# Optimization experiments

Measured on AMD Instinct MI355X. Metric: run time of the kernel, lower is better.

## Reference

```python
import jax, jax.numpy as jnp
import numpy as np

GW_EPS = 0.05
GW_SIGMA = 1.0
GW_OUTER_ITERS = 5
GW_SINK_ITERS = 20
N_HEADS = 8
EPS = 1e-8


def normalize_affinity(P):
    # symmetrize, scale to [0,1]
    P = 0.5 * (P + jnp.swapaxes(P, -1, -2))
    mx = jnp.max(P, axis=(-2, -1), keepdims=True)
    return P / jnp.maximum(mx, EPS)


def entropic_gw(C1, C2, a, b, eps, outer_iters, sink_iters):
    # C1: [B,H,S,S] node-space cost, C2: [B,H,K,K] slot-space cost
    # a: [B,H,S], b: [B,H,K] marginals. Square-loss entropic GW (Peyre et al.)
    T = a[..., :, None] * b[..., None, :]                      # [B,H,S,K]
    cC1 = jnp.einsum('bhij,bhj->bhi', C1 * C1, a)              # [B,H,S]
    cC2 = jnp.einsum('bhk,bhkl->bhl', b, C2 * C2)              # [B,H,K]
    const = cC1[..., :, None] + cC2[..., None, :]              # [B,H,S,K]
    tens = const
    for _ in range(outer_iters):
        tens = const - 2.0 * jnp.einsum('bhis,bhsk,bhlk->bhil', C1, T, C2)
        Kmat = jnp.exp(-tens / eps)
        u = jnp.ones_like(a)
        v = jnp.ones_like(b)
        def sink_step(carry, _):
            u, v = carry
            u = a / jnp.maximum(jnp.einsum('bhik,bhk->bhi', Kmat, v), 1e-30)
            v = b / jnp.maximum(jnp.einsum('bhik,bhi->bhk', Kmat, u), 1e-30)
            return (u, v), None
        (u, v), _ = jax.lax.scan(sink_step, (u, v), None, length=sink_iters)
        T = u[..., :, None] * Kmat * v[..., None, :]
    gw_val = jnp.sum(tens * T, axis=(-2, -1))                  # [B,H]
    return T, gw_val


def _forward(desc_embeddings, name_value_embeddings, shared_attn, prior_Q, DG, b, v_w, v_b):
    B, new_seq, D = name_value_embeddings.shape
    S = new_seq - 1
    H = N_HEADS
    hd = D // H

    # structural adjacency: CLS->Var on, Var->CLS off, Var-Var without self-loop
    var_adj = 1.0 - jnp.eye(S, dtype=name_value_embeddings.dtype)
    adj = jnp.zeros((new_seq, new_seq), dtype=name_value_embeddings.dtype)
    adj = adj.at[1:, 1:].set(var_adj)
    adj = adj.at[0, 1:].set(1.0)

    # Var-Var affinity from shared attention (detached in original)
    P_var = jax.lax.stop_gradient(shared_attn[:, :, 1:, 1:])   # [B,H,S,S]
    P_norm = normalize_affinity(P_var)
    DP = 1.0 - P_norm                                          # affinity -> distance

    deg_P = 0.5 * (P_norm.sum(-1) + P_norm.sum(-2))            # [B,H,S]
    a = deg_P / jnp.maximum(deg_P.sum(-1, keepdims=True), EPS)

    _, gw_val = entropic_gw(DP, DG, a, b, GW_EPS, GW_OUTER_ITERS, GW_SINK_ITERS)
    alpha = jnp.exp(-gw_val / GW_SIGMA)                        # [B,H] in (0,1]

    # sharpen prior Q by alpha (power sharpening + row renorm)
    Q_hat = jnp.power(jnp.maximum(prior_Q, EPS), 1.0 + alpha[..., None, None])
    Q_hat = Q_hat / jnp.maximum(Q_hat.sum(-1, keepdims=True), EPS)

    # embed Q_hat into CLS-augmented attention, mask, row-normalize
    slot = jnp.zeros((B, H, new_seq, new_seq), dtype=Q_hat.dtype)
    slot = slot.at[:, :, 1:, 1:].set(Q_hat)
    slot = slot.at[:, :, 0, 1:].set(1.0)
    slot = slot * adj[None, None]
    attn = slot / jnp.maximum(slot.sum(-1, keepdims=True), EPS)  # [B,H,S1,S1]

    v = name_value_embeddings @ v_w.T + v_b                    # [B,S1,D]
    v = v.reshape(B, new_seq, H, hd).transpose(0, 2, 1, 3)     # [B,H,S1,hd]
    context = jnp.einsum('bhij,bhjd->bhid', attn, v)
    basis_outputs = context.transpose(0, 2, 1, 3)              # [B,S1,H,hd]
    return basis_outputs, attn


def setup_inputs() -> dict:
    key = jax.random.key(0)
    ks = jax.random.split(key, 8)
    B, S1, D, H, K = 32, 385, 256, 8, 16
    S = S1 - 1
    desc = jax.random.normal(ks[0], (B, S, D), jnp.float32)
    nv = jax.random.normal(ks[1], (B, S1, D), jnp.float32)
    shared_attn = jax.nn.softmax(jax.random.normal(ks[2], (B, H, S1, S1), jnp.float32), axis=-1)
    prior_Q = jax.nn.softmax(jax.random.normal(ks[3], (B, H, S, S), jnp.float32), axis=-1)
    DG = jax.random.uniform(ks[4], (B, H, K, K), jnp.float32)
    DG = 0.5 * (DG + jnp.swapaxes(DG, -1, -2))
    b = jax.random.uniform(ks[5], (B, H, K), jnp.float32) + 0.1
    b = b / b.sum(-1, keepdims=True)
    v_w = jax.random.normal(ks[6], (D, D), jnp.float32) * (1.0 / np.sqrt(D))
    v_b = jnp.zeros((D,), jnp.float32)
    return {"desc_embeddings": desc, "name_value_embeddings": nv, "shared_attn": shared_attn,
            "prior_Q": prior_Q, "DG": DG, "b": b, "v_w": v_w, "v_b": v_b}


def reference(desc_embeddings, name_value_embeddings, shared_attn, prior_Q, DG, b, v_w, v_b):
    return _forward(desc_embeddings, name_value_embeddings, shared_attn, prior_Q, DG, b, v_w, v_b)
```

## Files before the change

kernel.cpp:

```cpp
#include <hip/hip_runtime.h>
#include <math.h>

constexpr int kS  = 384;
constexpr int kS1 = 385;
constexpr int kH  = 8;
constexpr int kB  = 32;
constexpr int kD  = 256;
constexpr float kEPS = 1e-8f;
constexpr float kNEG_INV_EPS_LOG2E = 28.853900817779268f;

__device__ __forceinline__ float waveReduceSum(float v) {
    #pragma unroll
    for (int m = 1; m < 64; m <<= 1) v += __shfl_xor(v, m);
    return v;
}
__device__ __forceinline__ float waveReduceMax(float v) {
    #pragma unroll
    for (int m = 1; m < 64; m <<= 1) v = fmaxf(v, __shfl_xor(v, m));
    return v;
}

__global__ __launch_bounds__(384) void k1_gw(
    const float* __restrict__ shared_attn,
    const float* __restrict__ DG,
    const float* __restrict__ bmarg,
    float* __restrict__ sym_ws,
    float* __restrict__ alpha_out)
{
    const int head = blockIdx.x;
    const int tid  = threadIdx.x;
    const int lane = tid & 63, wid = tid >> 6;

    __shared__ __align__(16) float uni[8320];
    __shared__ float Ks[kS * 17];
    __shared__ float ravu[kS];
    __shared__ float part[16 * 24];
    __shared__ float C2l[256];
    __shared__ float bl16[16], cb16[16], cC216[16], vls[16];
    __shared__ float wred[6];

    float* tA = uni;
    float* tB = uni + 4160;
    float* Ms = uni;

    const float* P = shared_attn + (size_t)head * (kS1 * kS1);
    float* SYM = sym_ws + (size_t)head * (kS1 * kS1);

    ravu[tid] = 0.f;
    if (tid < 256) C2l[tid] = DG[head * 256 + tid];
    if (tid >= 256 && tid < 272) bl16[tid - 256] = bmarg[head * 16 + (tid - 256)];
    __syncthreads();

    float mymax = -1e30f;
    for (int ti = 0; ti < 6; ++ti)
    for (int tj = ti; tj < 6; ++tj) {
        for (int e = tid; e < 4096; e += 384) {
            int r = e >> 6, c = e & 63;
            tA[r * 65 + c] = P[(ti * 64 + r + 1) * kS1 + (tj * 64 + c + 1)];
            tB[r * 65 + c] = P[(tj * 64 + r + 1) * kS1 + (ti * 64 + c + 1)];
        }
        __syncthreads();
        for (int e = tid; e < 4096; e += 384) {
            int r = e >> 6, c = e & 63;
            float v = 0.5f * (tA[r * 65 + c] + tB[c * 65 + r]);
            tA[r * 65 + c] = v;
            mymax = fmaxf(mymax, v);
        }
        __syncthreads();
        for (int e = tid; e < 4096; e += 384) {
            int r = e >> 6, c = e & 63;
            SYM[(ti * 64 + r) * kS + tj * 64 + c] = tA[r * 65 + c];
        }
        if (ti != tj) {
            for (int e = tid; e < 4096; e += 384) {
                int r = e >> 6, c = e & 63;
                SYM[(tj * 64 + r) * kS + ti * 64 + c] = tA[c * 65 + r];
            }
        }
        if (tid < 64) {
            int r = tid; float s = 0.f;
            #pragma unroll 8
            for (int c = 0; c < 64; ++c) s += tA[r * 65 + c];
            ravu[ti * 64 + r] += s;
        } else if (tid < 128 && ti != tj) {
            int c = tid - 64; float s = 0.f;
            #pragma unroll 8
            for (int r = 0; r < 64; ++r) s += tA[r * 65 + c];
            ravu[tj * 64 + c] += s;
        }
        __syncthreads();
    }

    float wm = waveReduceMax(mymax);
    if (lane == 0) wred[wid] = wm;
    __syncthreads();
    const float mx = fmaxf(fmaxf(fmaxf(wred[0], wred[1]), fmaxf(wred[2], wred[3])),
                           fmaxf(wred[4], wred[5]));
    float tloc = ravu[tid];
    float tw = waveReduceSum(tloc);
    __syncthreads();
    if (lane == 0) wred[wid] = tw;
    __syncthreads();
    const float total = wred[0] + wred[1] + wred[2] + wred[3] + wred[4] + wred[5];

    const float den_mx = fmaxf(mx, kEPS);
    const float inv_mx = 1.0f / den_mx;
    const float Sdeg   = total * inv_mx;
    const float den_a  = fmaxf(Sdeg, kEPS);
    const float a_reg  = (tloc * inv_mx) / den_a;
    __syncthreads();
    ravu[tid] = a_reg;

    if (tid < 16) {
        float cb = 0.f, cc2 = 0.f;
        #pragma unroll
        for (int k = 0; k < 16; ++k) {
            cb += bl16[k] * C2l[tid * 16 + k];
            float c2 = C2l[k * 16 + tid];
            cc2 = fmaf(bl16[k] * c2, c2, cc2);
        }
        cb16[tid] = cb; cC216[tid] = cc2;
    }
    __syncthreads();

    float t1 = 0.f, t2 = 0.f;
    {
        const float* symcol = SYM + tid;
        #pragma unroll 4
        for (int s = 0; s < kS; ++s) {
            float sym = symcol[s * kS];
            float dp  = fmaf(-inv_mx, sym, 1.0f);
            float as  = ravu[s];
            t1 = fmaf(dp, as, t1);
            t2 = fmaf(dp * dp, as, t2);
        }
    }
    const float cc1 = t2;
    #pragma unroll
    for (int l = 0; l < 16; ++l) {
        float tens = cc1 + cC216[l] - 2.0f * cb16[l] * t1;
        Ks[tid * 17 + l] = exp2f(tens * (-kNEG_INV_EPS_LOG2E));
    }

    float vreg[16];
    float u_i = 0.f;

    auto sinkhorn = [&]() {
        #pragma unroll
        for (int l = 0; l < 16; ++l) vreg[l] = 1.0f;
        for (int it = 0; it < 20; ++it) {
            float su = 0.f;
            #pragma unroll
            for (int l = 0; l < 16; ++l) su = fmaf(Ks[tid * 17 + l], vreg[l], su);
            u_i = a_reg / fmaxf(su, 1e-30f);
            ravu[tid] = u_i;
            __syncthreads();
            {
                int l = tid & 15, g = tid >> 4;
                float sv = 0.f;
                #pragma unroll
                for (int j = 0; j < 16; ++j)
                    sv = fmaf(Ks[(g * 16 + j) * 17 + l], ravu[g * 16 + j], sv);
                part[l * 24 + g] = sv;
            }
            __syncthreads();
            if (tid < 16) {
                float dn = 0.f;
                #pragma unroll
                for (int g = 0; g < 24; ++g) dn += part[tid * 24 + g];
                vls[tid] = bl16[tid] / fmaxf(dn, 1e-30f);
            }
            __syncthreads();
            #pragma unroll
            for (int l = 0; l < 16; ++l) vreg[l] = vls[l];
        }
    };

    __syncthreads();
    sinkhorn();

    float tens16[16];
    #pragma unroll
    for (int l = 0; l < 16; ++l) tens16[l] = 0.f;

    for (int outer = 1; outer < 5; ++outer) {
        {
            float wk[16];
            #pragma unroll
            for (int k = 0; k < 16; ++k) wk[k] = Ks[tid * 17 + k] * vreg[k];
            float m[16];
            #pragma unroll
            for (int l = 0; l < 16; ++l) {
                float acc = 0.f;
                #pragma unroll
                for (int k = 0; k < 16; ++k) acc = fmaf(wk[k], C2l[l * 16 + k], acc);
                m[l] = acc * u_i;
            }
            float4* Ms4 = (float4*)Ms;
            Ms4[tid * 4 + 0] = make_float4(m[0],  m[1],  m[2],  m[3]);
            Ms4[tid * 4 + 1] = make_float4(m[4],  m[5],  m[6],  m[7]);
            Ms4[tid * 4 + 2] = make_float4(m[8],  m[9],  m[10], m[11]);
            Ms4[tid * 4 + 3] = make_float4(m[12], m[13], m[14], m[15]);
        }
        __syncthreads();
        float rd[16];
        #pragma unroll
        for (int l = 0; l < 16; ++l) rd[l] = 0.f;
        {
            const float* symcol = SYM + tid;
            const float4* Ms4 = (const float4*)Ms;
            #pragma unroll 2
            for (int s = 0; s < kS; ++s) {
                float sym = symcol[s * kS];
                float dp  = fmaf(-inv_mx, sym, 1.0f);
                float4 m0 = Ms4[s * 4 + 0];
                float4 m1 = Ms4[s * 4 + 1];
                float4 m2 = Ms4[s * 4 + 2];
                float4 m3 = Ms4[s * 4 + 3];
                rd[0]  = fmaf(dp, m0.x, rd[0]);  rd[1]  = fmaf(dp, m0.y, rd[1]);
                rd[2]  = fmaf(dp, m0.z, rd[2]);  rd[3]  = fmaf(dp, m0.w, rd[3]);
                rd[4]  = fmaf(dp, m1.x, rd[4]);  rd[5]  = fmaf(dp, m1.y, rd[5]);
                rd[6]  = fmaf(dp, m1.z, rd[6]);  rd[7]  = fmaf(dp, m1.w, rd[7]);
                rd[8]  = fmaf(dp, m2.x, rd[8]);  rd[9]  = fmaf(dp, m2.y, rd[9]);
                rd[10] = fmaf(dp, m2.z, rd[10]); rd[11] = fmaf(dp, m2.w, rd[11]);
                rd[12] = fmaf(dp, m3.x, rd[12]); rd[13] = fmaf(dp, m3.y, rd[13]);
                rd[14] = fmaf(dp, m3.z, rd[14]); rd[15] = fmaf(dp, m3.w, rd[15]);
            }
        }
        #pragma unroll
        for (int l = 0; l < 16; ++l) {
            float tens = cc1 + cC216[l] - 2.0f * rd[l];
            if (outer == 4) tens16[l] = tens;
            Ks[tid * 17 + l] = exp2f(tens * (-kNEG_INV_EPS_LOG2E));
        }
        __syncthreads();
        sinkhorn();
    }

    float g = 0.f;
    #pragma unroll
    for (int l = 0; l < 16; ++l)
        g = fmaf(tens16[l] * Ks[tid * 17 + l], vreg[l], g);
    g *= u_i;
    float gww = waveReduceSum(g);
    __syncthreads();
    if (lane == 0) wred[wid] = gww;
    __syncthreads();
    if (tid == 0) {
        float gw = wred[0] + wred[1] + wred[2] + wred[3] + wred[4] + wred[5];
        alpha_out[head] = expf(-gw);
    }
}

__global__ __launch_bounds__(256) void k2_attn(
    const float* __restrict__ priorQ,
    const float* __restrict__ alpha_in,
    float* __restrict__ attn_out)
{
    const int tid  = threadIdx.x;
    const int lane = tid & 63, wid = tid >> 6;
    const int head = blockIdx.x / 97;
    const int i    = (blockIdx.x % 97) * 4 + wid;
    if (i >= kS1) return;
    float* row = attn_out + (size_t)head * (kS1 * kS1) + (size_t)i * kS1;
    if (i == 0) {
        const float val = 1.0f / 384.0f;
        for (int j = lane; j < kS1; j += 64) row[j] = (j == 0) ? 0.f : val;
        return;
    }
    const float e = 1.0f + alpha_in[head];
    const float* q = priorQ + (size_t)head * (kS * kS) + (size_t)(i - 1) * kS;
    float p[6];
    float loc = 0.f, locd = 0.f;
    #pragma unroll
    for (int k = 0; k < 6; ++k) {
        int j = lane + k * 64;
        float qv = fmaxf(q[j], kEPS);
        float pv = exp2f(e * log2f(qv));
        p[k] = pv;
        loc += pv;
        if (j == i - 1) locd = pv;
    }
    float sum = loc, pd = locd;
    #pragma unroll
    for (int m = 1; m < 64; m <<= 1) { sum += __shfl_xor(sum, m); pd += __shfl_xor(pd, m); }
    const float qsum  = fmaxf(sum, kEPS);
    const float srow  = (sum - pd) / qsum;
    const float scale = 1.0f / (qsum * fmaxf(srow, kEPS));
    if (lane == 0) row[0] = 0.f;
    #pragma unroll
    for (int k = 0; k < 6; ++k) {
        int j = lane + k * 64;
        row[1 + j] = (j == i - 1) ? 0.f : p[k] * scale;
    }
}

__global__ __launch_bounds__(256) void k3_vproj(
    const float* __restrict__ nv,
    const float* __restrict__ vw,
    const float* __restrict__ vb,
    float* __restrict__ vfull)
{
    __shared__ float At[64][17];
    __shared__ float Bt[256][17];
    const int tid = threadIdx.x;
    const int r0  = blockIdx.x * 64;
    const int tx  = tid & 31;
    const int ty  = tid >> 5;
    const int M   = kB * kS1;
    float acc[8][8];
    #pragma unroll
    for (int ri = 0; ri < 8; ++ri)
        #pragma unroll
        for (int ci = 0; ci < 8; ++ci) acc[ri][ci] = 0.f;

    for (int k0 = 0; k0 < 256; k0 += 16) {
        __syncthreads();
        for (int e = tid; e < 1024; e += 256) {
            int r = e >> 4, kk = e & 15;
            int rowi = r0 + r;
            At[r][kk] = (rowi < M) ? nv[rowi * 256 + k0 + kk] : 0.f;
        }
        for (int e = tid; e < 4096; e += 256) {
            int c = e >> 4, kk = e & 15;
            Bt[c][kk] = vw[c * 256 + k0 + kk];
        }
        __syncthreads();
        #pragma unroll
        for (int kk = 0; kk < 16; ++kk) {
            float av[8], bv[8];
            #pragma unroll
            for (int ri = 0; ri < 8; ++ri) av[ri] = At[ty * 8 + ri][kk];
            #pragma unroll
            for (int ci = 0; ci < 8; ++ci) bv[ci] = Bt[tx + 32 * ci][kk];
            #pragma unroll
            for (int ri = 0; ri < 8; ++ri)
                #pragma unroll
                for (int ci = 0; ci < 8; ++ci)
                    acc[ri][ci] = fmaf(av[ri], bv[ci], acc[ri][ci]);
        }
    }
    for (int ri = 0; ri < 8; ++ri) {
        int rowi = r0 + ty * 8 + ri;
        if (rowi < M) {
            #pragma unroll
            for (int ci = 0; ci < 8; ++ci) {
                int c = tx + 32 * ci;
                vfull[rowi * 256 + c] = acc[ri][ci] + vb[c];
            }
        }
    }
}

__global__ __launch_bounds__(256) void k4_ctx(
    const float* __restrict__ attn,
    const float* __restrict__ vfull,
    float* __restrict__ basis)
{
    __shared__ __align__(16) float at[8 * 32 * 28];
    __shared__ float vt[24 * 256];
    const int tid = threadIdx.x;
    const int bb  = blockIdx.y;
    const int i0  = blockIdx.x * 32;
    const int h   = tid >> 5;
    float acc[32];
    #pragma unroll
    for (int i = 0; i < 32; ++i) acc[i] = 0.f;
    const float* attnB = attn + (size_t)bb * kH * kS1 * kS1;
    const float* vB    = vfull + (size_t)bb * kS1 * 256;

    for (int j0 = 0; j0 < kS1; j0 += 24) {
        __syncthreads();
        for (int e = tid; e < 6144; e += 256) {
            int jj = e % 24, ii = (e / 24) & 31, hh = e / (24 * 32);
            int gi = i0 + ii, gj = j0 + jj;
            float v = (gi < kS1 && gj < kS1)
                      ? attnB[(size_t)hh * kS1 * kS1 + (size_t)gi * kS1 + gj] : 0.f;
            at[(hh * 32 + ii) * 28 + jj] = v;
        }
        for (int e = tid; e < 6144; e += 256) {
            int c = e & 255, jr = e >> 8;
            int gj = j0 + jr;
            vt[jr * 256 + c] = (gj < kS1) ? vB[gj * 256 + c] : 0.f;
        }
        __syncthreads();
        #pragma unroll
        for (int j4 = 0; j4 < 6; ++j4) {
            float v0 = vt[(j4 * 4 + 0) * 256 + tid];
            float v1 = vt[(j4 * 4 + 1) * 256 + tid];
            float v2 = vt[(j4 * 4 + 2) * 256 + tid];
            float v3 = vt[(j4 * 4 + 3) * 256 + tid];
            #pragma unroll
            for (int i = 0; i < 32; ++i) {
                float4 av = *(const float4*)&at[(h * 32 + i) * 28 + j4 * 4];
                acc[i] = fmaf(av.x, v0, fmaf(av.y, v1, fmaf(av.z, v2, fmaf(av.w, v3, acc[i]))));
            }
        }
    }
    for (int i = 0; i < 32; ++i) {
        int gi = i0 + i;
        if (gi < kS1) basis[((size_t)bb * kS1 + gi) * 256 + tid] = acc[i];
    }
}

extern "C" void kernel_launch(void* const* d_in, const int* in_sizes, int n_in,
                              void* d_out, int out_size, void* d_ws, size_t ws_size,
                              hipStream_t stream) {
    (void)in_sizes; (void)n_in; (void)out_size; (void)ws_size;
    const float* nv    = (const float*)d_in[1];
    const float* sattn = (const float*)d_in[2];
    const float* pq    = (const float*)d_in[3];
    const float* dg    = (const float*)d_in[4];
    const float* bm    = (const float*)d_in[5];
    const float* vw    = (const float*)d_in[6];
    const float* vb    = (const float*)d_in[7];

    float* out   = (float*)d_out;
    float* basis = out;
    float* attn  = out + (size_t)kB * kS1 * kD;
    float* alpha = (float*)d_ws;
    float* vfull = (float*)((char*)d_ws + 4096);

    k1_gw<<<256, 384, 0, stream>>>(sattn, dg, bm, attn, alpha);
    k2_attn<<<256 * 97, 256, 0, stream>>>(pq, alpha, attn);
    k3_vproj<<<193, 256, 0, stream>>>(nv, vw, vb, vfull);
    k4_ctx<<<dim3(13, 32), 256, 0, stream>>>(attn, vfull, basis);
}
```

Measured before the change: 1.334 ms.

## Split GW symmetrization into parallel kernel, keep Sinkhorn kernel in registers, retile context

Symmetrizing the affinity matrix, along with its row sums and max, moves out of the per-head GW kernel into a separate kernel launched with six blocks per head, so that phase no longer runs on only 256 blocks. The GW kernel now holds the Gibbs kernel in registers and reduces the Sinkhorn column sums with wave shuffles instead of a shared-memory pass. It also reads SYM rows as float4 rather than strided columns, which relies on SYM being symmetric and on a per-head alignment offset. Separately, the context kernel uses 16-row tiles for more blocks and loads V with float4. The cost is an extra launch plus storing and re-reading the sums and max through global memory.

New measurement: 1.322 ms. About the same (-0.9%).

```diff
diff --git a/kernel.cpp b/kernel.cpp
--- a/kernel.cpp
+++ b/kernel.cpp
@@ -20,8 +20,63 @@
     return v;
 }
 
-__global__ __launch_bounds__(384) void k1_gw(
+__device__ __forceinline__ size_t symBase(int head) {
+    return (size_t)head * (kS1 * kS1) + (size_t)((4 - (head & 3)) & 3);
+}
+
+__global__ __launch_bounds__(256) void k1a_sym(
     const float* __restrict__ shared_attn,
+    float* __restrict__ sym_ws)
+{
+    const int head = blockIdx.y;
+    const int ti   = blockIdx.x;
+    const int tid  = threadIdx.x;
+    const int c    = tid & 63;
+    const int w    = tid >> 6;
+
+    __shared__ float tB[64 * 65];
+    __shared__ float wredA[4];
+
+    const float* P = shared_attn + (size_t)head * (kS1 * kS1);
+    float* SYM = sym_ws + symBase(head);
+    float* rs  = SYM + kS * kS;
+    float* mxs = rs + kS;
+
+    float rs_part[16];
+    #pragma unroll
+    for (int k = 0; k < 16; ++k) rs_part[k] = 0.f;
+    float mymax = 0.f;
+
+    for (int tj = 0; tj < 6; ++tj) {
+        __syncthreads();
+        for (int e = tid; e < 4096; e += 256) {
+            int r = e >> 6, cc = e & 63;
+            tB[r * 65 + cc] = P[(size_t)(1 + tj * 64 + r) * kS1 + (1 + ti * 64 + cc)];
+        }
+        __syncthreads();
+        #pragma unroll
+        for (int k = 0; k < 16; ++k) {
+            int r = w + 4 * k;
+            float av = P[(size_t)(1 + ti * 64 + r) * kS1 + (1 + tj * 64 + c)];
+            float v  = 0.5f * (av + tB[c * 65 + r]);
+            mymax = fmaxf(mymax, v);
+            rs_part[k] += v;
+            SYM[(size_t)(ti * 64 + r) * kS + tj * 64 + c] = v;
+        }
+    }
+    #pragma unroll
+    for (int k = 0; k < 16; ++k) {
+        float s = waveReduceSum(rs_part[k]);
+        if (c == 0) rs[ti * 64 + w + 4 * k] = s;
+    }
+    float wm = waveReduceMax(mymax);
+    if (c == 0) wredA[w] = wm;
+    __syncthreads();
+    if (tid == 0)
+        mxs[ti] = fmaxf(fmaxf(wredA[0], wredA[1]), fmaxf(wredA[2], wredA[3]));
+}
+
+__global__ __launch_bounds__(384) void k1b_gw(
     const float* __restrict__ DG,
     const float* __restrict__ bmarg,
     float* __restrict__ sym_ws,
@@ -31,84 +86,32 @@
     const int tid  = threadIdx.x;
     const int lane = tid & 63, wid = tid >> 6;
 
-    __shared__ __align__(16) float uni[8320];
-    __shared__ float Ks[kS * 17];
+    __shared__ __align__(16) float Ms[kS * 16];
     __shared__ float ravu[kS];
-    __shared__ float part[16 * 24];
+    __shared__ float part[6 * 16];
     __shared__ float C2l[256];
     __shared__ float bl16[16], cb16[16], cC216[16], vls[16];
     __shared__ float wred[6];
 
-    float* tA = uni;
-    float* tB = uni + 4160;
-    float* Ms = uni;
-
-    const float* P = shared_attn + (size_t)head * (kS1 * kS1);
-    float* SYM = sym_ws + (size_t)head * (kS1 * kS1);
-
-    ravu[tid] = 0.f;
+    float* SYM = sym_ws + symBase(head);
+    const float* rs  = SYM + kS * kS;
+    const float* mxp = rs + kS;
+
     if (tid < 256) C2l[tid] = DG[head * 256 + tid];
     if (tid >= 256 && tid < 272) bl16[tid - 256] = bmarg[head * 16 + (tid - 256)];
-    __syncthreads();
-
-    float mymax = -1e30f;
-    for (int ti = 0; ti < 6; ++ti)
-    for (int tj = ti; tj < 6; ++tj) {
-        for (int e = tid; e < 4096; e += 384) {
-            int r = e >> 6, c = e & 63;
-            tA[r * 65 + c] = P[(ti * 64 + r + 1) * kS1 + (tj * 64 + c + 1)];
-            tB[r * 65 + c] = P[(tj * 64 + r + 1) * kS1 + (ti * 64 + c + 1)];
-        }
-        __syncthreads();
-        for (int e = tid; e < 4096; e += 384) {
-            int r = e >> 6, c = e & 63;
-            float v = 0.5f * (tA[r * 65 + c] + tB[c * 65 + r]);
-            tA[r * 65 + c] = v;
-            mymax = fmaxf(mymax, v);
-        }
-        __syncthreads();
-        for (int e = tid; e < 4096; e += 384) {
-            int r = e >> 6, c = e & 63;
-            SYM[(ti * 64 + r) * kS + tj * 64 + c] = tA[r * 65 + c];
-        }
-        if (ti != tj) {
-            for (int e = tid; e < 4096; e += 384) {
-                int r = e >> 6, c = e & 63;
-                SYM[(tj * 64 + r) * kS + ti * 64 + c] = tA[c * 65 + r];
-            }
-        }
-        if (tid < 64) {
-            int r = tid; float s = 0.f;
-            #pragma unroll 8
-            for (int c = 0; c < 64; ++c) s += tA[r * 65 + c];
-            ravu[ti * 64 + r] += s;
-        } else if (tid < 128 && ti != tj) {
-            int c = tid - 64; float s = 0.f;
-            #pragma unroll 8
-            for (int r = 0; r < 64; ++r) s += tA[r * 65 + c];
-            ravu[tj * 64 + c] += s;
-        }
-        __syncthreads();
-    }
-
-    float wm = waveReduceMax(mymax);
-    if (lane == 0) wred[wid] = wm;
-    __syncthreads();
-    const float mx = fmaxf(fmaxf(fmaxf(wred[0], wred[1]), fmaxf(wred[2], wred[3])),
-                           fmaxf(wred[4], wred[5]));
-    float tloc = ravu[tid];
+
+    const float tloc = rs[tid];
     float tw = waveReduceSum(tloc);
-    __syncthreads();
     if (lane == 0) wred[wid] = tw;
     __syncthreads();
     const float total = wred[0] + wred[1] + wred[2] + wred[3] + wred[4] + wred[5];
-
+    const float mx = fmaxf(fmaxf(fmaxf(mxp[0], mxp[1]), fmaxf(mxp[2], mxp[3])),
+                           fmaxf(mxp[4], mxp[5]));
     const float den_mx = fmaxf(mx, kEPS);
     const float inv_mx = 1.0f / den_mx;
     const float Sdeg   = total * inv_mx;
     const float den_a  = fmaxf(Sdeg, kEPS);
     const float a_reg  = (tloc * inv_mx) / den_a;
-    __syncthreads();
     ravu[tid] = a_reg;
 
     if (tid < 16) {
@@ -123,27 +126,25 @@
     }
     __syncthreads();
 
+    const float4* __restrict__ symrow = (const float4*)(SYM + (size_t)tid * kS);
     float t1 = 0.f, t2 = 0.f;
-    {
-        const float* symcol = SYM + tid;
-        #pragma unroll 4
-        for (int s = 0; s < kS; ++s) {
-            float sym = symcol[s * kS];
-            float dp  = fmaf(-inv_mx, sym, 1.0f);
-            float as  = ravu[s];
-            t1 = fmaf(dp, as, t1);
-            t2 = fmaf(dp * dp, as, t2);
-        }
+    #pragma unroll 4
+    for (int s4 = 0; s4 < 96; ++s4) {
+        float4 v4 = symrow[s4];
+        const float* av = &ravu[s4 * 4];
+        float dp;
+        dp = fmaf(-inv_mx, v4.x, 1.0f); t1 = fmaf(dp, av[0], t1); t2 = fmaf(dp * dp, av[0], t2);
+        dp = fmaf(-inv_mx, v4.y, 1.0f); t1 = fmaf(dp, av[1], t1); t2 = fmaf(dp * dp, av[1], t2);
+        dp = fmaf(-inv_mx, v4.z, 1.0f); t1 = fmaf(dp, av[2], t1); t2 = fmaf(dp * dp, av[2], t2);
+        dp = fmaf(-inv_mx, v4.w, 1.0f); t1 = fmaf(dp, av[3], t1); t2 = fmaf(dp * dp, av[3], t2);
     }
     const float cc1 = t2;
-    #pragma unroll
-    for (int l = 0; l < 16; ++l) {
-        float tens = cc1 + cC216[l] - 2.0f * cb16[l] * t1;
-        Ks[tid * 17 + l] = exp2f(tens * (-kNEG_INV_EPS_LOG2E));
-    }
-
-    float vreg[16];
+
+    float kreg[16], vreg[16];
     float u_i = 0.f;
+    #pragma unroll
+    for (int l = 0; l < 16; ++l)
+        kreg[l] = exp2f((cc1 + cC216[l] - 2.0f * cb16[l] * t1) * (-kNEG_INV_EPS_LOG2E));
 
     auto sinkhorn = [&]() {
         #pragma unroll
@@ -151,23 +152,17 @@
         for (int it = 0; it < 20; ++it) {
             float su = 0.f;
             #pragma unroll
-            for (int l = 0; l < 16; ++l) su = fmaf(Ks[tid * 17 + l], vreg[l], su);
+            for (int l = 0; l < 16; ++l) su = fmaf(kreg[l], vreg[l], su);
             u_i = a_reg / fmaxf(su, 1e-30f);
-            ravu[tid] = u_i;
-            __syncthreads();
-            {
-                int l = tid & 15, g = tid >> 4;
-                float sv = 0.f;
-                #pragma unroll
-                for (int j = 0; j < 16; ++j)
-                    sv = fmaf(Ks[(g * 16 + j) * 17 + l], ravu[g * 16 + j], sv);
-                part[l * 24 + g] = sv;
+            #pragma unroll
+            for (int l = 0; l < 16; ++l) {
+                float t = waveReduceSum(kreg[l] * u_i);
+                if (lane == 0) part[wid * 16 + l] = t;
             }
             __syncthreads();
             if (tid < 16) {
-                float dn = 0.f;
-                #pragma unroll
-                for (int g = 0; g < 24; ++g) dn += part[tid * 24 + g];
+                float dn = part[tid] + part[16 + tid] + part[32 + tid] +
+                           part[48 + tid] + part[64 + tid] + part[80 + tid];
                 vls[tid] = bl16[tid] / fmaxf(dn, 1e-30f);
             }
             __syncthreads();
@@ -176,7 +171,6 @@
         }
     };
 
-    __syncthreads();
     sinkhorn();
 
     float tens16[16];
@@ -187,7 +181,7 @@
         {
             float wk[16];
             #pragma unroll
-            for (int k = 0; k < 16; ++k) wk[k] = Ks[tid * 17 + k] * vreg[k];
+            for (int k = 0; k < 16; ++k) wk[k] = kreg[k] * vreg[k];
             float m[16];
             #pragma unroll
             for (int l = 0; l < 16; ++l) {
@@ -196,54 +190,55 @@
                 for (int k = 0; k < 16; ++k) acc = fmaf(wk[k], C2l[l * 16 + k], acc);
                 m[l] = acc * u_i;
             }
-            float4* Ms4 = (float4*)Ms;
-            Ms4[tid * 4 + 0] = make_float4(m[0],  m[1],  m[2],  m[3]);
-            Ms4[tid * 4 + 1] = make_float4(m[4],  m[5],  m[6],  m[7]);
-            Ms4[tid * 4 + 2] = make_float4(m[8],  m[9],  m[10], m[11]);
-            Ms4[tid * 4 + 3] = make_float4(m[12], m[13], m[14], m[15]);
+            float4* Ms4w = (float4*)Ms;
+            Ms4w[tid * 4 + 0] = make_float4(m[0],  m[1],  m[2],  m[3]);
+            Ms4w[tid * 4 + 1] = make_float4(m[4],  m[5],  m[6],  m[7]);
+            Ms4w[tid * 4 + 2] = make_float4(m[8],  m[9],  m[10], m[11]);
+            Ms4w[tid * 4 + 3] = make_float4(m[12], m[13], m[14], m[15]);
         }
         __syncthreads();
         float rd[16];
         #pragma unroll
         for (int l = 0; l < 16; ++l) rd[l] = 0.f;
         {
-            const float* symcol = SYM + tid;
             const float4* Ms4 = (const float4*)Ms;
             #pragma unroll 2
-            for (int s = 0; s < kS; ++s) {
-                float sym = symcol[s * kS];
-                float dp  = fmaf(-inv_mx, sym, 1.0f);
-                float4 m0 = Ms4[s * 4 + 0];
-                float4 m1 = Ms4[s * 4 + 1];
-                float4 m2 = Ms4[s * 4 + 2];
-                float4 m3 = Ms4[s * 4 + 3];
-                rd[0]  = fmaf(dp, m0.x, rd[0]);  rd[1]  = fmaf(dp, m0.y, rd[1]);
-                rd[2]  = fmaf(dp, m0.z, rd[2]);  rd[3]  = fmaf(dp, m0.w, rd[3]);
-                rd[4]  = fmaf(dp, m1.x, rd[4]);  rd[5]  = fmaf(dp, m1.y, rd[5]);
-                rd[6]  = fmaf(dp, m1.z, rd[6]);  rd[7]  = fmaf(dp, m1.w, rd[7]);
-                rd[8]  = fmaf(dp, m2.x, rd[8]);  rd[9]  = fmaf(dp, m2.y, rd[9]);
-                rd[10] = fmaf(dp, m2.z, rd[10]); rd[11] = fmaf(dp, m2.w, rd[11]);
-                rd[12] = fmaf(dp, m3.x, rd[12]); rd[13] = fmaf(dp, m3.y, rd[13]);
-                rd[14] = fmaf(dp, m3.z, rd[14]); rd[15] = fmaf(dp, m3.w, rd[15]);
+            for (int s4 = 0; s4 < 96; ++s4) {
+                float4 v4 = symrow[s4];
+                #pragma unroll
+                for (int j = 0; j < 4; ++j) {
+                    float sym = (j == 0) ? v4.x : (j == 1) ? v4.y : (j == 2) ? v4.z : v4.w;
+                    float dp = fmaf(-inv_mx, sym, 1.0f);
+                    const int s = s4 * 4 + j;
+                    float4 m0 = Ms4[s * 4 + 0];
+                    float4 m1 = Ms4[s * 4 + 1];
+                    float4 m2 = Ms4[s * 4 + 2];
+                    float4 m3 = Ms4[s * 4 + 3];
+                    rd[0]  = fmaf(dp, m0.x, rd[0]);  rd[1]  = fmaf(dp, m0.y, rd[1]);
+                    rd[2]  = fmaf(dp, m0.z, rd[2]);  rd[3]  = fmaf(dp, m0.w, rd[3]);
+                    rd[4]  = fmaf(dp, m1.x, rd[4]);  rd[5]  = fmaf(dp, m1.y, rd[5]);
+                    rd[6]  = fmaf(dp, m1.z, rd[6]);  rd[7]  = fmaf(dp, m1.w, rd[7]);
+                    rd[8]  = fmaf(dp, m2.x, rd[8]);  rd[9]  = fmaf(dp, m2.y, rd[9]);
+                    rd[10] = fmaf(dp, m2.z, rd[10]); rd[11] = fmaf(dp, m2.w, rd[11]);
+                    rd[12] = fmaf(dp, m3.x, rd[12]); rd[13] = fmaf(dp, m3.y, rd[13]);
+                    rd[14] = fmaf(dp, m3.z, rd[14]); rd[15] = fmaf(dp, m3.w, rd[15]);
+                }
             }
         }
         #pragma unroll
         for (int l = 0; l < 16; ++l) {
             float tens = cc1 + cC216[l] - 2.0f * rd[l];
             if (outer == 4) tens16[l] = tens;
-            Ks[tid * 17 + l] = exp2f(tens * (-kNEG_INV_EPS_LOG2E));
-        }
-        __syncthreads();
+            kreg[l] = exp2f(tens * (-kNEG_INV_EPS_LOG2E));
+        }
         sinkhorn();
     }
 
     float g = 0.f;
     #pragma unroll
-    for (int l = 0; l < 16; ++l)
-        g = fmaf(tens16[l] * Ks[tid * 17 + l], vreg[l], g);
+    for (int l = 0; l < 16; ++l) g = fmaf(tens16[l] * kreg[l], vreg[l], g);
     g *= u_i;
     float gww = waveReduceSum(g);
-    __syncthreads();
     if (lane == 0) wred[wid] = gww;
     __syncthreads();
     if (tid == 0) {
@@ -357,47 +352,49 @@
     const float* __restrict__ vfull,
     float* __restrict__ basis)
 {
-    __shared__ __align__(16) float at[8 * 32 * 28];
-    __shared__ float vt[24 * 256];
+    __shared__ __align__(16) float at[8 * 16 * 36];
+    __shared__ __align__(16) float vt[32 * 256];
     const int tid = threadIdx.x;
     const int bb  = blockIdx.y;
-    const int i0  = blockIdx.x * 32;
+    const int i0  = blockIdx.x * 16;
     const int h   = tid >> 5;
-    float acc[32];
-    #pragma unroll
-    for (int i = 0; i < 32; ++i) acc[i] = 0.f;
+    float acc[16];
+    #pragma unroll
+    for (int i = 0; i < 16; ++i) acc[i] = 0.f;
     const float* attnB = attn + (size_t)bb * kH * kS1 * kS1;
     const float* vB    = vfull + (size_t)bb * kS1 * 256;
 
-    for (int j0 = 0; j0 < kS1; j0 += 24) {
-        __syncthreads();
-        for (int e = tid; e < 6144; e += 256) {
-            int jj = e % 24, ii = (e / 24) & 31, hh = e / (24 * 32);
+    for (int j0 = 0; j0 < kS1; j0 += 32) {
+        __syncthreads();
+        for (int e = tid; e < 4096; e += 256) {
+            int jj = e & 31, ii = (e >> 5) & 15, hh = e >> 9;
             int gi = i0 + ii, gj = j0 + jj;
-            float v = (gi < kS1 && gj < kS1)
-                      ? attnB[(size_t)hh * kS1 * kS1 + (size_t)gi * kS1 + gj] : 0.f;
-            at[(hh * 32 + ii) * 28 + jj] = v;
-        }
-        for (int e = tid; e < 6144; e += 256) {
-            int c = e & 255, jr = e >> 8;
+            at[(hh * 16 + ii) * 36 + jj] = (gi < kS1 && gj < kS1)
+                ? attnB[(size_t)hh * kS1 * kS1 + (size_t)gi * kS1 + gj] : 0.f;
+        }
+        for (int e = tid; e < 2048; e += 256) {
+            int c4 = e & 63, jr = e >> 6;
             int gj = j0 + jr;
-            vt[jr * 256 + c] = (gj < kS1) ? vB[gj * 256 + c] : 0.f;
-        }
-        __syncthreads();
-        #pragma unroll
-        for (int j4 = 0; j4 < 6; ++j4) {
+            float4 vv = (gj < kS1) ? *(const float4*)&vB[(size_t)gj * 256 + c4 * 4]
+                                   : make_float4(0.f, 0.f, 0.f, 0.f);
+            *(float4*)&vt[jr * 256 + c4 * 4] = vv;
+        }
+        __syncthreads();
+        #pragma unroll
+        for (int j4 = 0; j4 < 8; ++j4) {
             float v0 = vt[(j4 * 4 + 0) * 256 + tid];
             float v1 = vt[(j4 * 4 + 1) * 256 + tid];
             float v2 = vt[(j4 * 4 + 2) * 256 + tid];
             float v3 = vt[(j4 * 4 + 3) * 256 + tid];
             #pragma unroll
-            for (int i = 0; i < 32; ++i) {
-                float4 av = *(const float4*)&at[(h * 32 + i) * 28 + j4 * 4];
+            for (int i = 0; i < 16; ++i) {
+                float4 av = *(const float4*)&at[(h * 16 + i) * 36 + j4 * 4];
                 acc[i] = fmaf(av.x, v0, fmaf(av.y, v1, fmaf(av.z, v2, fmaf(av.w, v3, acc[i]))));
             }
         }
     }
-    for (int i = 0; i < 32; ++i) {
+    #pragma unroll
+    for (int i = 0; i < 16; ++i) {
         int gi = i0 + i;
         if (gi < kS1) basis[((size_t)bb * kS1 + gi) * 256 + tid] = acc[i];
     }
@@ -421,8 +418,9 @@
     float* alpha = (float*)d_ws;
     float* vfull = (float*)((char*)d_ws + 4096);
 
-    k1_gw<<<256, 384, 0, stream>>>(sattn, dg, bm, attn, alpha);
+    k1a_sym<<<dim3(6, 256), 256, 0, stream>>>(sattn, attn);
+    k1b_gw<<<256, 384, 0, stream>>>(dg, bm, attn, alpha);
     k2_attn<<<256 * 97, 256, 0, stream>>>(pq, alpha, attn);
     k3_vproj<<<193, 256, 0, stream>>>(nv, vw, vb, vfull);
-    k4_ctx<<<dim3(13, 32), 256, 0, stream>>>(attn, vfull, basis);
-}
+    k4_ctx<<<dim3(25, 32), 256, 0, stream>>>(attn, vfull, basis);
+}
```
